# Performance work log

Hardware: AMD Instinct MI355X
Metric: run time of the kernel (lower is better)

The kernel has to match this reference:

```python
import jax, jax.numpy as jnp
import numpy as np

K_BITS = 128  # hash bits (k in __init__)
WORD = 32     # pack bits into uint32 words -> K_BITS // WORD = 4 words


def _pack_bits(bits_u32):
    # bits_u32: [N, K_BITS] uint32 in {0,1} -> [N, K_BITS//WORD] uint32 keys
    N = bits_u32.shape[0]
    b = bits_u32.reshape(N, K_BITS // WORD, WORD)
    shifts = jnp.arange(WORD, dtype=jnp.uint32)
    return jnp.sum(jnp.left_shift(b, shifts), axis=-1, dtype=jnp.uint32)  # [N, 4]


def setup_inputs() -> dict:
    key = jax.random.key(0)
    k1, k2 = jax.random.split(key)
    T, B, D = 128, 64, 4096
    latent_state = jax.random.normal(k1, (T, B, D), dtype=jnp.float32)
    A = jax.random.normal(k2, (K_BITS, D), dtype=jnp.float32)  # fixed random projection buffer
    return {"latent_state": latent_state, "A": A}


def reference(latent_state, A):
    # latent_state: [T, B, D]; A: [k, D]. Returns intrinsic reward [T, B].
    T, B, D = latent_state.shape
    flat = latent_state.reshape(T * B, D)                    # detach is a no-op for fwd
    proj = flat @ A.T                                        # [N, k]
    bits = (proj > 0).astype(jnp.uint32)                     # SimHash sign bits
    words = _pack_bits(bits)                                 # [N, 4] collision-free 128-bit key

    # counts dict starts empty each run: visit count of row i is the number of
    # rows j <= i with an identical key (keys processed in row order).
    N = words.shape[0]
    eq = jnp.ones((N, N), dtype=bool)
    for w in range(K_BITS // WORD):  # small fixed loop over 4 key words
        eq = eq & (words[:, None, w] == words[None, :, w])
    counts = jnp.tril(eq).sum(axis=1)                        # [N] int, >= 1
    intrinsic = 1.0 / jnp.sqrt(counts.astype(latent_state.dtype))
    return intrinsic.reshape(T, B)
```

## Files before the change

kernel.cpp:

```cpp
#include <hip/hip_runtime.h>
#include <stdint.h>

#define D_DIM 4096
#define N_ROWS 8192

typedef __attribute__((ext_vector_type(8))) short bfrag8;
typedef __attribute__((ext_vector_type(4))) float facc4;
typedef unsigned long long u64;

__device__ __forceinline__ uint32_t pack_bf16x2(float lo, float hi) {
    union { float f; uint32_t u; } a, b;
    a.f = lo; b.f = hi;
    return (b.u & 0xFFFF0000u) | (a.u >> 16);
}

__global__ void __launch_bounds__(256)
prep_A(const float* __restrict__ A, uint32_t* __restrict__ Bimg) {
    const int S = blockIdx.x * 256 + threadIdx.x;
    const int chunk = S >> 10;
    const int rest  = S & 1023;
    const int tks   = rest >> 6;
    const int lane  = rest & 63;
    const int t  = tks >> 1;
    const int ks = tks & 1;
    const int c  = lane & 15;
    const int q  = lane >> 4;
    const float* src = A + (size_t)(16 * t + c) * D_DIM + chunk * 64 + ks * 32 + q * 8;
    float4 f0 = *(const float4*)(src);
    float4 f1 = *(const float4*)(src + 4);
    uint4 o;
    o.x = pack_bf16x2(f0.x, f0.y);
    o.y = pack_bf16x2(f0.z, f0.w);
    o.z = pack_bf16x2(f1.x, f1.y);
    o.w = pack_bf16x2(f1.z, f1.w);
    *(uint4*)(Bimg + (size_t)S * 4) = o;
}

__global__ void __launch_bounds__(256, 3)
gemm_direct(const float* __restrict__ L, const uint32_t* __restrict__ Bimg,
            float* __restrict__ partials, int kpb) {
    const int tid  = threadIdx.x;
    const int lane = tid & 63;
    const int gw   = blockIdx.x * 4 + (tid >> 6);
    const int split = gw >> 9;
    const int mwave = gw & 511;
    const int c = lane & 15;
    const int q = lane >> 4;

    const float* lrow = L + (size_t)(16 * mwave + c) * D_DIM;

    facc4 acc[8];
#pragma unroll
    for (int t = 0; t < 8; t++) acc[t] = (facc4){0.f, 0.f, 0.f, 0.f};

    const int k0 = split * kpb;
#pragma unroll 2
    for (int k = k0; k < k0 + kpb; k++) {
        const int kc = k * 64;
        bfrag8 a[2];
#pragma unroll
        for (int ks = 0; ks < 2; ks++) {
            const float* p = lrow + kc + ks * 32 + q * 8;
            float4 f0 = *(const float4*)(p);
            float4 f1 = *(const float4*)(p + 4);
            uint4 u;
            u.x = pack_bf16x2(f0.x, f0.y);
            u.y = pack_bf16x2(f0.z, f0.w);
            u.z = pack_bf16x2(f1.x, f1.y);
            u.w = pack_bf16x2(f1.z, f1.w);
            a[ks] = *(bfrag8*)&u;
        }
        const uint32_t* bbase = Bimg + ((size_t)k * 16) * 256 + lane * 4;
#pragma unroll
        for (int t = 0; t < 8; t++) {
#pragma unroll
            for (int ks = 0; ks < 2; ks++) {
                bfrag8 b = *(const bfrag8*)(bbase + (t * 2 + ks) * 256);
                acc[t] = __builtin_amdgcn_mfma_f32_16x16x32_bf16(a[ks], b, acc[t], 0, 0, 0);
            }
        }
    }

    float* P = partials + (size_t)split * N_ROWS * 128 + (size_t)(16 * mwave) * 128;
#pragma unroll
    for (int t = 0; t < 8; t++)
#pragma unroll
        for (int r = 0; r < 4; r++)
            P[(4 * q + r) * 128 + 16 * t + c] = acc[t][r];
}

__global__ void __launch_bounds__(256)
reduce_pack(const float* __restrict__ partials, u64* __restrict__ folded, int S) {
    const int row  = blockIdx.x * 4 + (threadIdx.x >> 6);
    const int lane = threadIdx.x & 63;
    float s0 = 0.f, s1 = 0.f;
    for (int s = 0; s < S; s++) {
        const float* P = partials + ((size_t)s * N_ROWS * 128) + (size_t)row * 128;
        s0 += P[lane];
        s1 += P[lane + 64];
    }
    u64 b0 = __ballot(s0 > 0.0f);
    u64 b1 = __ballot(s1 > 0.0f);
    if (lane == 0) folded[row] = b0 ^ b1;
}

__global__ void __launch_bounds__(256)
count_rows(const u64* __restrict__ folded, float* __restrict__ out) {
    __shared__ u64 K[N_ROWS];
    const int tid = threadIdx.x;
    for (int i = tid; i < N_ROWS / 2; i += 256)
        ((uint4*)K)[i] = ((const uint4*)folded)[i];
    __syncthreads();

    const int g    = blockIdx.x * 4 + (tid >> 6);
    const int lane = tid & 63;
    int rows[4];
    u64 my[4];
    int cnt[4] = {0, 0, 0, 0};
#pragma unroll
    for (int r = 0; r < 4; r++) {
        rows[r] = g + 2048 * r;
        my[r] = K[rows[r]];
    }
    const int maxrow = rows[3];
    for (int j = lane; j <= maxrow; j += 64) {
        u64 k = K[j];
#pragma unroll
        for (int r = 0; r < 4; r++)
            cnt[r] += (int)((j <= rows[r]) & (k == my[r]));
    }
#pragma unroll
    for (int r = 0; r < 4; r++) {
        int v = cnt[r];
#pragma unroll
        for (int o = 32; o; o >>= 1) v += __shfl_xor(v, o, 64);
        if (lane == 0) out[rows[r]] = rsqrtf((float)v);
    }
}

extern "C" void kernel_launch(void* const* d_in, const int* in_sizes, int n_in,
                              void* d_out, int out_size, void* d_ws, size_t ws_size,
                              hipStream_t stream) {
    const float* latent = (const float*)d_in[0];
    const float* A      = (const float*)d_in[1];
    float* out          = (float*)d_out;

    uint32_t* Bimg = (uint32_t*)d_ws;
    u64* folded = (u64*)((char*)d_ws + (1 << 20));
    float* partials = (float*)((char*)d_ws + (1 << 20) + (1 << 16));

    const size_t base = (1 << 20) + (1 << 16);
    const size_t per_split = (size_t)N_ROWS * 128 * sizeof(float);
    int S = 1;
    if (ws_size >= base + 8 * per_split)      S = 8;
    else if (ws_size >= base + 4 * per_split) S = 4;
    else if (ws_size >= base + 2 * per_split) S = 2;

    prep_A<<<256, 256, 0, stream>>>(A, Bimg);
    gemm_direct<<<128 * S, 256, 0, stream>>>(latent, Bimg, partials, 64 / S);
    reduce_pack<<<2048, 256, 0, stream>>>(partials, folded, S);
    count_rows<<<512, 256, 0, stream>>>(folded, out);
}
```

Baseline: 240.9 us.

## Pre-convert latent to bf16 in a separate pass before the GEMM

Adds a kernel that converts the whole fp32 latent tensor to a packed bf16 copy in workspace. A new GEMM variant then loads ready-made bf16 fragments directly instead of loading fp32 and packing inside the MFMA loop. This removes conversion ALU work and halves the GEMM's A-operand traffic. In exchange it adds an extra full read of the 128MB input plus a 64MB write and re-read, and needs a large workspace, falling back to the old path if the workspace is too small.

```diff
diff --git a/kernel.cpp b/kernel.cpp
--- a/kernel.cpp
+++ b/kernel.cpp
@@ -36,6 +36,63 @@
     *(uint4*)(Bimg + (size_t)S * 4) = o;
 }
 
+__global__ void __launch_bounds__(256)
+copy_bf16(const float* __restrict__ L, uint32_t* __restrict__ Lb) {
+    const size_t total  = (size_t)N_ROWS * D_DIM / 8;
+    const size_t stride = (size_t)gridDim.x * 256;
+    for (size_t i = blockIdx.x * 256 + threadIdx.x; i < total; i += stride) {
+        const float* p = L + i * 8;
+        float4 f0 = *(const float4*)(p);
+        float4 f1 = *(const float4*)(p + 4);
+        uint4 o;
+        o.x = pack_bf16x2(f0.x, f0.y);
+        o.y = pack_bf16x2(f0.z, f0.w);
+        o.z = pack_bf16x2(f1.x, f1.y);
+        o.w = pack_bf16x2(f1.z, f1.w);
+        *(uint4*)(Lb + i * 4) = o;
+    }
+}
+
+__global__ void __launch_bounds__(256)
+gemm_direct_b(const uint32_t* __restrict__ Lb, const uint32_t* __restrict__ Bimg,
+              float* __restrict__ partials, int kpb) {
+    const int tid  = threadIdx.x;
+    const int lane = tid & 63;
+    const int gw   = blockIdx.x * 4 + (tid >> 6);
+    const int split = gw >> 9;
+    const int mwave = gw & 511;
+    const int c = lane & 15;
+    const int q = lane >> 4;
+    const uint32_t* lrow = Lb + (size_t)(16 * mwave + c) * (D_DIM / 2) + q * 4;
+
+    facc4 acc[8];
+#pragma unroll
+    for (int t = 0; t < 8; t++) acc[t] = (facc4){0.f, 0.f, 0.f, 0.f};
+
+    const int k0 = split * kpb;
+#pragma unroll 2
+    for (int k = k0; k < k0 + kpb; k++) {
+        const int kc = k * 32;
+        bfrag8 a0 = *(const bfrag8*)(lrow + kc);
+        bfrag8 a1 = *(const bfrag8*)(lrow + kc + 16);
+        const uint32_t* bbase = Bimg + ((size_t)k * 16) * 256 + lane * 4;
+#pragma unroll
+        for (int t = 0; t < 8; t++) {
+            bfrag8 b0 = *(const bfrag8*)(bbase + (t * 2 + 0) * 256);
+            acc[t] = __builtin_amdgcn_mfma_f32_16x16x32_bf16(a0, b0, acc[t], 0, 0, 0);
+            bfrag8 b1 = *(const bfrag8*)(bbase + (t * 2 + 1) * 256);
+            acc[t] = __builtin_amdgcn_mfma_f32_16x16x32_bf16(a1, b1, acc[t], 0, 0, 0);
+        }
+    }
+
+    float* P = partials + (size_t)split * N_ROWS * 128 + (size_t)(16 * mwave) * 128;
+#pragma unroll
+    for (int t = 0; t < 8; t++)
+#pragma unroll
+        for (int r = 0; r < 4; r++)
+            P[(4 * q + r) * 128 + 16 * t + c] = acc[t][r];
+}
+
 __global__ void __launch_bounds__(256, 3)
 gemm_direct(const float* __restrict__ L, const uint32_t* __restrict__ Bimg,
             float* __restrict__ partials, int kpb) {
@@ -46,7 +103,6 @@
     const int mwave = gw & 511;
     const int c = lane & 15;
     const int q = lane >> 4;
-
     const float* lrow = L + (size_t)(16 * mwave + c) * D_DIM;
 
     facc4 acc[8];
@@ -80,7 +136,6 @@
             }
         }
     }
-
     float* P = partials + (size_t)split * N_ROWS * 128 + (size_t)(16 * mwave) * 128;
 #pragma unroll
     for (int t = 0; t < 8; t++)
@@ -145,19 +200,31 @@
     const float* A      = (const float*)d_in[1];
     float* out          = (float*)d_out;
 
+    const size_t OFF_FOLDED = (size_t)1 << 20;
+    const size_t OFF_LB     = OFF_FOLDED + ((size_t)1 << 16);
+    const size_t OFF_PART   = OFF_LB + ((size_t)64 << 20);
+    const size_t NEED       = OFF_PART + ((size_t)32 << 20);
+
     uint32_t* Bimg = (uint32_t*)d_ws;
-    u64* folded = (u64*)((char*)d_ws + (1 << 20));
-    float* partials = (float*)((char*)d_ws + (1 << 20) + (1 << 16));
-
-    const size_t base = (1 << 20) + (1 << 16);
-    const size_t per_split = (size_t)N_ROWS * 128 * sizeof(float);
-    int S = 1;
-    if (ws_size >= base + 8 * per_split)      S = 8;
-    else if (ws_size >= base + 4 * per_split) S = 4;
-    else if (ws_size >= base + 2 * per_split) S = 2;
+    u64* folded    = (u64*)((char*)d_ws + OFF_FOLDED);
 
     prep_A<<<256, 256, 0, stream>>>(A, Bimg);
-    gemm_direct<<<128 * S, 256, 0, stream>>>(latent, Bimg, partials, 64 / S);
-    reduce_pack<<<2048, 256, 0, stream>>>(partials, folded, S);
+
+    if (ws_size >= NEED) {
+        uint32_t* Lb    = (uint32_t*)((char*)d_ws + OFF_LB);
+        float* partials = (float*)((char*)d_ws + OFF_PART);
+        copy_bf16<<<2048, 256, 0, stream>>>(latent, Lb);
+        gemm_direct_b<<<128 * 8, 256, 0, stream>>>(Lb, Bimg, partials, 64 / 8);
+        reduce_pack<<<2048, 256, 0, stream>>>(partials, folded, 8);
+    } else {
+        float* partials = (float*)((char*)d_ws + OFF_LB);
+        const size_t per_split = (size_t)N_ROWS * 128 * sizeof(float);
+        int S = 1;
+        if (ws_size >= OFF_LB + 8 * per_split)      S = 8;
+        else if (ws_size >= OFF_LB + 4 * per_split) S = 4;
+        else if (ws_size >= OFF_LB + 2 * per_split) S = 2;
+        gemm_direct<<<128 * S, 256, 0, stream>>>(latent, Bimg, partials, 64 / S);
+        reduce_pack<<<2048, 256, 0, stream>>>(partials, folded, S);
+    }
     count_rows<<<512, 256, 0, stream>>>(folded, out);
 }
```

Measured after the change: 259.8 us. +7.8%, slower.
